# Optimization experiments

Measured on AMD Instinct MI355X. Metric: run time of the kernel, lower is better.

## Reference

```python
import jax, jax.numpy as jnp
import numpy as np

B, H, S, D = 2, 16, 2048, 64


def setup_inputs() -> dict:
    key = jax.random.key(0)
    kq, kk, kv = jax.random.split(key, 3)
    q = jax.random.normal(kq, (B, H, S, D), dtype=jnp.float32)
    k = jax.random.normal(kk, (B, H, S, D), dtype=jnp.float32)
    v = jax.random.normal(kv, (B, H, S, D), dtype=jnp.float32)
    # causal mask, broadcast over heads: True = keep
    mask = jnp.broadcast_to(jnp.tril(jnp.ones((S, S), dtype=bool)), (B, 1, S, S))
    return {"q": q, "k": k, "v": v, "mask": mask}


def reference(q, k, v, mask):
    d_k = q.shape[-1]
    scale = 1.0 / jnp.sqrt(jnp.asarray(d_k, dtype=q.dtype))
    # [B,H,S,S] scores = q @ k^T / sqrt(d_k)
    scores = jnp.einsum("bhqd,bhkd->bhqk", q, k) * scale
    scores = jnp.where(mask, scores, jnp.asarray(-jnp.inf, dtype=scores.dtype))
    attn = jax.nn.softmax(scores, axis=-1)
    # dropout is identity in eval mode (reference baseline)
    out = jnp.einsum("bhqk,bhkd->bhqd", attn, v)
    return out, attn
```

## Files before the change

### kernel.cpp

```cpp
#include <hip/hip_runtime.h>
#include <hip/hip_bf16.h>


#define SLEN 2048
#define DHEAD 64
#define QT 64
#define KT 64
#define LDP 72

typedef __attribute__((ext_vector_type(8))) short short8;
typedef __attribute__((ext_vector_type(4))) float f32x4;

__device__ __forceinline__ unsigned short f2b(float x) {
    __hip_bfloat16 h = __float2bfloat16(x);
    return __builtin_bit_cast(unsigned short, h);
}

__global__ __launch_bounds__(256, 4) void attn_fused_kernel(
    const float* __restrict__ qg,
    const float* __restrict__ kg,
    const float* __restrict__ vg,
    float* __restrict__ outg,
    float* __restrict__ attng)
{
    const int qt   = blockIdx.x;
    const int bh   = blockIdx.y;
    const int tid  = threadIdx.x;
    const int w    = tid >> 6;
    const int lane = tid & 63;
    const int m    = lane & 15;
    const int quad = lane >> 4;

    const int q0 = qt * QT;
    const size_t bh_qkv = (size_t)bh * SLEN * DHEAD;
    const float* qb = qg + bh_qkv;
    const float* kb = kg + bh_qkv;
    const float* vb = vg + bh_qkv;
    float* outb  = outg + bh_qkv;
    float* attnb = attng + (size_t)bh * SLEN * SLEN;

    __shared__ unsigned short Qs[QT][LDP];
    __shared__ unsigned short Ks[KT][LDP];
    __shared__ unsigned short VTs[DHEAD][LDP];
    __shared__ unsigned short Ps[4][16][LDP];

    for (int i = tid; i < QT * 16; i += 256) {
        int row = i >> 4;
        int c4  = (i & 15) << 2;
        float4 f = *(const float4*)(qb + (size_t)(q0 + row) * DHEAD + c4);
        uint2 pk;
        pk.x = (unsigned)f2b(f.x) | ((unsigned)f2b(f.y) << 16);
        pk.y = (unsigned)f2b(f.z) | ((unsigned)f2b(f.w) << 16);
        *(uint2*)&Qs[row][c4] = pk;
    }
    __syncthreads();

    short8 aQ0 = *(const short8*)&Qs[w * 16 + m][quad * 8];
    short8 aQ1 = *(const short8*)&Qs[w * 16 + m][32 + quad * 8];

    const float scale = 0.125f;
    const int qrow_base = q0 + w * 16 + quad * 4;

    float mx[4] = {-1e30f, -1e30f, -1e30f, -1e30f};
    float ls[4] = {0.f, 0.f, 0.f, 0.f};

    for (int kt = 0; kt <= qt; ++kt) {
        __syncthreads();
        for (int i = tid; i < KT * 16; i += 256) {
            int row = i >> 4;
            int c4  = (i & 15) << 2;
            float4 f = *(const float4*)(kb + (size_t)(kt * KT + row) * DHEAD + c4);
            uint2 pk;
            pk.x = (unsigned)f2b(f.x) | ((unsigned)f2b(f.y) << 16);
            pk.y = (unsigned)f2b(f.z) | ((unsigned)f2b(f.w) << 16);
            *(uint2*)&Ks[row][c4] = pk;
        }
        __syncthreads();

        float s[4][4];
#pragma unroll
        for (int ct = 0; ct < 4; ++ct) {
            f32x4 acc = {0.f, 0.f, 0.f, 0.f};
            short8 b0 = *(const short8*)&Ks[ct * 16 + m][quad * 8];
            short8 b1 = *(const short8*)&Ks[ct * 16 + m][32 + quad * 8];
            acc = __builtin_amdgcn_mfma_f32_16x16x32_bf16(aQ0, b0, acc, 0, 0, 0);
            acc = __builtin_amdgcn_mfma_f32_16x16x32_bf16(aQ1, b1, acc, 0, 0, 0);
            int key = kt * KT + ct * 16 + m;
#pragma unroll
            for (int r = 0; r < 4; ++r) {
                float sv = acc[r] * scale;
                if (key > qrow_base + r) sv = -1e30f;
                s[ct][r] = sv;
            }
        }
#pragma unroll
        for (int r = 0; r < 4; ++r) {
            float tm = fmaxf(fmaxf(s[0][r], s[1][r]), fmaxf(s[2][r], s[3][r]));
            tm = fmaxf(tm, __shfl_xor(tm, 1));
            tm = fmaxf(tm, __shfl_xor(tm, 2));
            tm = fmaxf(tm, __shfl_xor(tm, 4));
            tm = fmaxf(tm, __shfl_xor(tm, 8));
            float mn = fmaxf(mx[r], tm);
            float sum = __expf(s[0][r] - mn) + __expf(s[1][r] - mn) +
                        __expf(s[2][r] - mn) + __expf(s[3][r] - mn);
            sum += __shfl_xor(sum, 1);
            sum += __shfl_xor(sum, 2);
            sum += __shfl_xor(sum, 4);
            sum += __shfl_xor(sum, 8);
            ls[r] = ls[r] * __expf(mx[r] - mn) + sum;
            mx[r] = mn;
        }
    }

    float rl[4];
#pragma unroll
    for (int r = 0; r < 4; ++r) rl[r] = 1.0f / ls[r];

    f32x4 oacc[4];
#pragma unroll
    for (int nt = 0; nt < 4; ++nt) oacc[nt] = (f32x4){0.f, 0.f, 0.f, 0.f};

    for (int kt = 0; kt <= qt; ++kt) {
        __syncthreads();
        for (int i = tid; i < KT * 16; i += 256) {
            int row = i >> 4;
            int c4  = (i & 15) << 2;
            float4 f = *(const float4*)(kb + (size_t)(kt * KT + row) * DHEAD + c4);
            uint2 pk;
            pk.x = (unsigned)f2b(f.x) | ((unsigned)f2b(f.y) << 16);
            pk.y = (unsigned)f2b(f.z) | ((unsigned)f2b(f.w) << 16);
            *(uint2*)&Ks[row][c4] = pk;
            float4 fv = *(const float4*)(vb + (size_t)(kt * KT + row) * DHEAD + c4);
            VTs[c4 + 0][row] = f2b(fv.x);
            VTs[c4 + 1][row] = f2b(fv.y);
            VTs[c4 + 2][row] = f2b(fv.z);
            VTs[c4 + 3][row] = f2b(fv.w);
        }
        __syncthreads();

#pragma unroll
        for (int ct = 0; ct < 4; ++ct) {
            f32x4 acc = {0.f, 0.f, 0.f, 0.f};
            short8 b0 = *(const short8*)&Ks[ct * 16 + m][quad * 8];
            short8 b1 = *(const short8*)&Ks[ct * 16 + m][32 + quad * 8];
            acc = __builtin_amdgcn_mfma_f32_16x16x32_bf16(aQ0, b0, acc, 0, 0, 0);
            acc = __builtin_amdgcn_mfma_f32_16x16x32_bf16(aQ1, b1, acc, 0, 0, 0);
            int key = kt * KT + ct * 16 + m;
#pragma unroll
            for (int r = 0; r < 4; ++r) {
                int qrow = qrow_base + r;
                float p = 0.0f;
                if (key <= qrow) p = __expf(acc[r] * scale - mx[r]) * rl[r];
                attnb[(size_t)qrow * SLEN + key] = p;
                Ps[w][quad * 4 + r][ct * 16 + m] = f2b(p);
            }
        }

        short8 aP0 = *(const short8*)&Ps[w][m][quad * 8];
        short8 aP1 = *(const short8*)&Ps[w][m][32 + quad * 8];
#pragma unroll
        for (int nt = 0; nt < 4; ++nt) {
            short8 b0 = *(const short8*)&VTs[nt * 16 + m][quad * 8];
            short8 b1 = *(const short8*)&VTs[nt * 16 + m][32 + quad * 8];
            oacc[nt] = __builtin_amdgcn_mfma_f32_16x16x32_bf16(aP0, b0, oacc[nt], 0, 0, 0);
            oacc[nt] = __builtin_amdgcn_mfma_f32_16x16x32_bf16(aP1, b1, oacc[nt], 0, 0, 0);
        }
    }

#pragma unroll
    for (int nt = 0; nt < 4; ++nt)
#pragma unroll
        for (int r = 0; r < 4; ++r)
            outb[(size_t)(qrow_base + r) * DHEAD + nt * 16 + m] = oacc[nt][r];

    const int kend = (qt + 1) * KT;
    const int nz4 = (SLEN - kend) >> 2;
    const float4 z4 = {0.f, 0.f, 0.f, 0.f};
    for (int row = 0; row < QT; ++row) {
        float4* rp = (float4*)(attnb + (size_t)(q0 + row) * SLEN + kend);
        for (int i = tid; i < nz4; i += 256) rp[i] = z4;
    }
}

extern "C" void kernel_launch(void* const* d_in, const int* in_sizes, int n_in,
                              void* d_out, int out_size, void* d_ws, size_t ws_size,
                              hipStream_t stream) {
    const float* q = (const float*)d_in[0];
    const float* k = (const float*)d_in[1];
    const float* v = (const float*)d_in[2];
    float* out  = (float*)d_out;
    float* attn = out + (size_t)2 * 16 * 2048 * 64;

    dim3 grid(32, 32);
    attn_fused_kernel<<<grid, 256, 0, stream>>>(q, k, v, out, attn);
}
```

Measured before the change: 807.5 us.

## Double-buffer K/V tiles with register prefetch and single barrier per iteration

Prefetches the next K (and V) tile into registers while computing the current tile, storing into an alternate shared-memory buffer so only one barrier per iteration is needed. Reuses the Q shared buffer for the P tile to fit the extra buffers, and lowers the launch-bounds occupancy hint from 4 to 3. This aims to hide global load latency, at the cost of more registers and shared memory and possibly fewer resident blocks.

```diff
diff --git a/kernel.cpp b/kernel.cpp
--- a/kernel.cpp
+++ b/kernel.cpp
@@ -16,7 +16,14 @@
     return __builtin_bit_cast(unsigned short, h);
 }
 
-__global__ __launch_bounds__(256, 4) void attn_fused_kernel(
+__device__ __forceinline__ uint2 pack4(float4 f) {
+    uint2 pk;
+    pk.x = (unsigned)f2b(f.x) | ((unsigned)f2b(f.y) << 16);
+    pk.y = (unsigned)f2b(f.z) | ((unsigned)f2b(f.w) << 16);
+    return pk;
+}
+
+__global__ __launch_bounds__(256, 3) void attn_fused_kernel(
     const float* __restrict__ qg,
     const float* __restrict__ kg,
     const float* __restrict__ vg,
@@ -39,24 +46,23 @@
     float* outb  = outg + bh_qkv;
     float* attnb = attng + (size_t)bh * SLEN * SLEN;
 
-    __shared__ unsigned short Qs[QT][LDP];
-    __shared__ unsigned short Ks[KT][LDP];
-    __shared__ unsigned short VTs[DHEAD][LDP];
-    __shared__ unsigned short Ps[4][16][LDP];
-
-    for (int i = tid; i < QT * 16; i += 256) {
-        int row = i >> 4;
-        int c4  = (i & 15) << 2;
-        float4 f = *(const float4*)(qb + (size_t)(q0 + row) * DHEAD + c4);
-        uint2 pk;
-        pk.x = (unsigned)f2b(f.x) | ((unsigned)f2b(f.y) << 16);
-        pk.y = (unsigned)f2b(f.z) | ((unsigned)f2b(f.w) << 16);
-        *(uint2*)&Qs[row][c4] = pk;
+    __shared__ unsigned short QP[QT * LDP];
+    __shared__ unsigned short Ks[2][KT][LDP];
+    __shared__ unsigned short VTs[2][DHEAD][LDP];
+
+    const int rbase = tid >> 4;
+    const int cbase = (tid & 15) << 2;
+
+#pragma unroll
+    for (int j = 0; j < 4; ++j) {
+        int row = rbase + j * 16;
+        float4 f = *(const float4*)(qb + (size_t)(q0 + row) * DHEAD + cbase);
+        *(uint2*)&QP[row * LDP + cbase] = pack4(f);
     }
     __syncthreads();
 
-    short8 aQ0 = *(const short8*)&Qs[w * 16 + m][quad * 8];
-    short8 aQ1 = *(const short8*)&Qs[w * 16 + m][32 + quad * 8];
+    short8 aQ0 = *(const short8*)&QP[(w * 16 + m) * LDP + quad * 8];
+    short8 aQ1 = *(const short8*)&QP[(w * 16 + m) * LDP + 32 + quad * 8];
 
     const float scale = 0.125f;
     const int qrow_base = q0 + w * 16 + quad * 4;
@@ -64,106 +70,146 @@
     float mx[4] = {-1e30f, -1e30f, -1e30f, -1e30f};
     float ls[4] = {0.f, 0.f, 0.f, 0.f};
 
-    for (int kt = 0; kt <= qt; ++kt) {
+    {
+        float4 kf[4];
+#pragma unroll
+        for (int j = 0; j < 4; ++j)
+            kf[j] = *(const float4*)(kb + (size_t)(rbase + j * 16) * DHEAD + cbase);
+#pragma unroll
+        for (int j = 0; j < 4; ++j)
+            *(uint2*)&Ks[0][rbase + j * 16][cbase] = pack4(kf[j]);
         __syncthreads();
-        for (int i = tid; i < KT * 16; i += 256) {
-            int row = i >> 4;
-            int c4  = (i & 15) << 2;
-            float4 f = *(const float4*)(kb + (size_t)(kt * KT + row) * DHEAD + c4);
-            uint2 pk;
-            pk.x = (unsigned)f2b(f.x) | ((unsigned)f2b(f.y) << 16);
-            pk.y = (unsigned)f2b(f.z) | ((unsigned)f2b(f.w) << 16);
-            *(uint2*)&Ks[row][c4] = pk;
+
+        for (int kt = 0; kt <= qt; ++kt) {
+            const int cur = kt & 1;
+            float4 nf[4];
+            if (kt < qt) {
+#pragma unroll
+                for (int j = 0; j < 4; ++j)
+                    nf[j] = *(const float4*)(kb + (size_t)((kt + 1) * KT + rbase + j * 16) * DHEAD + cbase);
+            }
+
+            float s[4][4];
+#pragma unroll
+            for (int ct = 0; ct < 4; ++ct) {
+                f32x4 acc = {0.f, 0.f, 0.f, 0.f};
+                short8 b0 = *(const short8*)&Ks[cur][ct * 16 + m][quad * 8];
+                short8 b1 = *(const short8*)&Ks[cur][ct * 16 + m][32 + quad * 8];
+                acc = __builtin_amdgcn_mfma_f32_16x16x32_bf16(aQ0, b0, acc, 0, 0, 0);
+                acc = __builtin_amdgcn_mfma_f32_16x16x32_bf16(aQ1, b1, acc, 0, 0, 0);
+                int key = kt * KT + ct * 16 + m;
+#pragma unroll
+                for (int r = 0; r < 4; ++r) {
+                    float sv = acc[r] * scale;
+                    if (key > qrow_base + r) sv = -1e30f;
+                    s[ct][r] = sv;
+                }
+            }
+#pragma unroll
+            for (int r = 0; r < 4; ++r) {
+                float tm = fmaxf(fmaxf(s[0][r], s[1][r]), fmaxf(s[2][r], s[3][r]));
+                tm = fmaxf(tm, __shfl_xor(tm, 1));
+                tm = fmaxf(tm, __shfl_xor(tm, 2));
+                tm = fmaxf(tm, __shfl_xor(tm, 4));
+                tm = fmaxf(tm, __shfl_xor(tm, 8));
+                float mn = fmaxf(mx[r], tm);
+                float sum = __expf(s[0][r] - mn) + __expf(s[1][r] - mn) +
+                            __expf(s[2][r] - mn) + __expf(s[3][r] - mn);
+                sum += __shfl_xor(sum, 1);
+                sum += __shfl_xor(sum, 2);
+                sum += __shfl_xor(sum, 4);
+                sum += __shfl_xor(sum, 8);
+                ls[r] = ls[r] * __expf(mx[r] - mn) + sum;
+                mx[r] = mn;
+            }
+
+            if (kt < qt) {
+#pragma unroll
+                for (int j = 0; j < 4; ++j)
+                    *(uint2*)&Ks[cur ^ 1][rbase + j * 16][cbase] = pack4(nf[j]);
+            }
+            __syncthreads();
+        }
+    }
+
+    float rl[4];
+#pragma unroll
+    for (int r = 0; r < 4; ++r) rl[r] = 1.0f / ls[r];
+
+    f32x4 oacc[4];
+#pragma unroll
+    for (int nt = 0; nt < 4; ++nt) oacc[nt] = (f32x4){0.f, 0.f, 0.f, 0.f};
+
+    {
+        float4 kf[4], vf[4];
+#pragma unroll
+        for (int j = 0; j < 4; ++j) {
+            kf[j] = *(const float4*)(kb + (size_t)(rbase + j * 16) * DHEAD + cbase);
+            vf[j] = *(const float4*)(vb + (size_t)(rbase + j * 16) * DHEAD + cbase);
+        }
+#pragma unroll
+        for (int j = 0; j < 4; ++j) {
+            int row = rbase + j * 16;
+            *(uint2*)&Ks[0][row][cbase] = pack4(kf[j]);
+            VTs[0][cbase + 0][row] = f2b(vf[j].x);
+            VTs[0][cbase + 1][row] = f2b(vf[j].y);
+            VTs[0][cbase + 2][row] = f2b(vf[j].z);
+            VTs[0][cbase + 3][row] = f2b(vf[j].w);
         }
         __syncthreads();
 
-        float s[4][4];
-#pragma unroll
-        for (int ct = 0; ct < 4; ++ct) {
-            f32x4 acc = {0.f, 0.f, 0.f, 0.f};
-            short8 b0 = *(const short8*)&Ks[ct * 16 + m][quad * 8];
-            short8 b1 = *(const short8*)&Ks[ct * 16 + m][32 + quad * 8];
-            acc = __builtin_amdgcn_mfma_f32_16x16x32_bf16(aQ0, b0, acc, 0, 0, 0);
-            acc = __builtin_amdgcn_mfma_f32_16x16x32_bf16(aQ1, b1, acc, 0, 0, 0);
-            int key = kt * KT + ct * 16 + m;
-#pragma unroll
-            for (int r = 0; r < 4; ++r) {
-                float sv = acc[r] * scale;
-                if (key > qrow_base + r) sv = -1e30f;
-                s[ct][r] = sv;
-            }
-        }
-#pragma unroll
-        for (int r = 0; r < 4; ++r) {
-            float tm = fmaxf(fmaxf(s[0][r], s[1][r]), fmaxf(s[2][r], s[3][r]));
-            tm = fmaxf(tm, __shfl_xor(tm, 1));
-            tm = fmaxf(tm, __shfl_xor(tm, 2));
-            tm = fmaxf(tm, __shfl_xor(tm, 4));
-            tm = fmaxf(tm, __shfl_xor(tm, 8));
-            float mn = fmaxf(mx[r], tm);
-            float sum = __expf(s[0][r] - mn) + __expf(s[1][r] - mn) +
-                        __expf(s[2][r] - mn) + __expf(s[3][r] - mn);
-            sum += __shfl_xor(sum, 1);
-            sum += __shfl_xor(sum, 2);
-            sum += __shfl_xor(sum, 4);
-            sum += __shfl_xor(sum, 8);
-            ls[r] = ls[r] * __expf(mx[r] - mn) + sum;
-            mx[r] = mn;
-        }
-    }
-
-    float rl[4];
-#pragma unroll
-    for (int r = 0; r < 4; ++r) rl[r] = 1.0f / ls[r];
-
-    f32x4 oacc[4];
-#pragma unroll
-    for (int nt = 0; nt < 4; ++nt) oacc[nt] = (f32x4){0.f, 0.f, 0.f, 0.f};
-
-    for (int kt = 0; kt <= qt; ++kt) {
-        __syncthreads();
-        for (int i = tid; i < KT * 16; i += 256) {
-            int row = i >> 4;
-            int c4  = (i & 15) << 2;
-            float4 f = *(const float4*)(kb + (size_t)(kt * KT + row) * DHEAD + c4);
-            uint2 pk;
-            pk.x = (unsigned)f2b(f.x) | ((unsigned)f2b(f.y) << 16);
-            pk.y = (unsigned)f2b(f.z) | ((unsigned)f2b(f.w) << 16);
-            *(uint2*)&Ks[row][c4] = pk;
-            float4 fv = *(const float4*)(vb + (size_t)(kt * KT + row) * DHEAD + c4);
-            VTs[c4 + 0][row] = f2b(fv.x);
-            VTs[c4 + 1][row] = f2b(fv.y);
-            VTs[c4 + 2][row] = f2b(fv.z);
-            VTs[c4 + 3][row] = f2b(fv.w);
-        }
-        __syncthreads();
-
-#pragma unroll
-        for (int ct = 0; ct < 4; ++ct) {
-            f32x4 acc = {0.f, 0.f, 0.f, 0.f};
-            short8 b0 = *(const short8*)&Ks[ct * 16 + m][quad * 8];
-            short8 b1 = *(const short8*)&Ks[ct * 16 + m][32 + quad * 8];
-            acc = __builtin_amdgcn_mfma_f32_16x16x32_bf16(aQ0, b0, acc, 0, 0, 0);
-            acc = __builtin_amdgcn_mfma_f32_16x16x32_bf16(aQ1, b1, acc, 0, 0, 0);
-            int key = kt * KT + ct * 16 + m;
-#pragma unroll
-            for (int r = 0; r < 4; ++r) {
-                int qrow = qrow_base + r;
-                float p = 0.0f;
-                if (key <= qrow) p = __expf(acc[r] * scale - mx[r]) * rl[r];
-                attnb[(size_t)qrow * SLEN + key] = p;
-                Ps[w][quad * 4 + r][ct * 16 + m] = f2b(p);
-            }
-        }
-
-        short8 aP0 = *(const short8*)&Ps[w][m][quad * 8];
-        short8 aP1 = *(const short8*)&Ps[w][m][32 + quad * 8];
-#pragma unroll
-        for (int nt = 0; nt < 4; ++nt) {
-            short8 b0 = *(const short8*)&VTs[nt * 16 + m][quad * 8];
-            short8 b1 = *(const short8*)&VTs[nt * 16 + m][32 + quad * 8];
-            oacc[nt] = __builtin_amdgcn_mfma_f32_16x16x32_bf16(aP0, b0, oacc[nt], 0, 0, 0);
-            oacc[nt] = __builtin_amdgcn_mfma_f32_16x16x32_bf16(aP1, b1, oacc[nt], 0, 0, 0);
+        for (int kt = 0; kt <= qt; ++kt) {
+            const int cur = kt & 1;
+            float4 nk[4], nv[4];
+            if (kt < qt) {
+#pragma unroll
+                for (int j = 0; j < 4; ++j) {
+                    size_t roff = (size_t)((kt + 1) * KT + rbase + j * 16) * DHEAD + cbase;
+                    nk[j] = *(const float4*)(kb + roff);
+                    nv[j] = *(const float4*)(vb + roff);
+                }
+            }
+
+#pragma unroll
+            for (int ct = 0; ct < 4; ++ct) {
+                f32x4 acc = {0.f, 0.f, 0.f, 0.f};
+                short8 b0 = *(const short8*)&Ks[cur][ct * 16 + m][quad * 8];
+                short8 b1 = *(const short8*)&Ks[cur][ct * 16 + m][32 + quad * 8];
+                acc = __builtin_amdgcn_mfma_f32_16x16x32_bf16(aQ0, b0, acc, 0, 0, 0);
+                acc = __builtin_amdgcn_mfma_f32_16x16x32_bf16(aQ1, b1, acc, 0, 0, 0);
+                int key = kt * KT + ct * 16 + m;
+#pragma unroll
+                for (int r = 0; r < 4; ++r) {
+                    int qrow = qrow_base + r;
+                    float p = 0.0f;
+                    if (key <= qrow) p = __expf(acc[r] * scale - mx[r]) * rl[r];
+                    attnb[(size_t)qrow * SLEN + key] = p;
+                    QP[(w * 16 + quad * 4 + r) * LDP + ct * 16 + m] = f2b(p);
+                }
+            }
+
+            short8 aP0 = *(const short8*)&QP[(w * 16 + m) * LDP + quad * 8];
+            short8 aP1 = *(const short8*)&QP[(w * 16 + m) * LDP + 32 + quad * 8];
+#pragma unroll
+            for (int nt = 0; nt < 4; ++nt) {
+                short8 b0 = *(const short8*)&VTs[cur][nt * 16 + m][quad * 8];
+                short8 b1 = *(const short8*)&VTs[cur][nt * 16 + m][32 + quad * 8];
+                oacc[nt] = __builtin_amdgcn_mfma_f32_16x16x32_bf16(aP0, b0, oacc[nt], 0, 0, 0);
+                oacc[nt] = __builtin_amdgcn_mfma_f32_16x16x32_bf16(aP1, b1, oacc[nt], 0, 0, 0);
+            }
+
+            if (kt < qt) {
+#pragma unroll
+                for (int j = 0; j < 4; ++j) {
+                    int row = rbase + j * 16;
+                    *(uint2*)&Ks[cur ^ 1][row][cbase] = pack4(nk[j]);
+                    VTs[cur ^ 1][cbase + 0][row] = f2b(nv[j].x);
+                    VTs[cur ^ 1][cbase + 1][row] = f2b(nv[j].y);
+                    VTs[cur ^ 1][cbase + 2][row] = f2b(nv[j].z);
+                    VTs[cur ^ 1][cbase + 3][row] = f2b(nv[j].w);
+                }
+            }
+            __syncthreads();
         }
     }
 
```

After: 809.6 us. No clear change (+0.3%).
